# Optimization experiments

Measured on AMD Instinct MI355X. Metric: run time of the kernel, lower is better.

Reference implementation:

```python
import jax, jax.numpy as jnp
import numpy as np

OVERLAP_THRESH = 0.5
NEG_POS_RATIO = 3
VARIANCE = (0.1, 0.2)


def point_form(boxes):
    # center-size (cx,cy,w,h) -> corner (xmin,ymin,xmax,ymax)
    return jnp.concatenate([boxes[:, :2] - boxes[:, 2:] / 2,
                            boxes[:, :2] + boxes[:, 2:] / 2], axis=1)


def jaccard(a, b):
    # a: [O,4] corner boxes, b: [P,4] corner boxes -> IoU [O,P]
    lt = jnp.maximum(a[:, None, :2], b[None, :, :2])
    rb = jnp.minimum(a[:, None, 2:], b[None, :, 2:])
    wh = jnp.clip(rb - lt, 0.0)
    inter = wh[..., 0] * wh[..., 1]
    area_a = (a[:, 2] - a[:, 0]) * (a[:, 3] - a[:, 1])
    area_b = (b[:, 2] - b[:, 0]) * (b[:, 3] - b[:, 1])
    return inter / (area_a[:, None] + area_b[None, :] - inter)


def match_one(truths, priors):
    # truths: [O,4] corner form; priors: [P,4] center-size form
    O = truths.shape[0]
    overlaps = jaccard(truths, point_form(priors))          # [O,P]
    best_prior_idx = jnp.argmax(overlaps, axis=1)           # [O]
    best_truth_overlap = jnp.max(overlaps, axis=0)          # [P]
    best_truth_idx = jnp.argmax(overlaps, axis=0)           # [P]
    # force-assign each gt its best prior
    best_truth_overlap = best_truth_overlap.at[best_prior_idx].set(2.0)
    best_truth_idx = best_truth_idx.at[best_prior_idx].set(jnp.arange(O))
    matches = truths[best_truth_idx]                        # [P,4]
    # ARM: labels are all zeros -> conf = 0 + 1 = 1 for matched, 0 otherwise
    conf = jnp.where(best_truth_overlap < OVERLAP_THRESH, 0, 1).astype(jnp.int32)
    # encode(matched, priors, variances)
    g_cxcy = ((matches[:, :2] + matches[:, 2:]) / 2 - priors[:, :2]) / (VARIANCE[0] * priors[:, 2:])
    g_wh = jnp.log((matches[:, 2:] - matches[:, :2]) / priors[:, 2:]) / VARIANCE[1]
    loc = jnp.concatenate([g_cxcy, g_wh], axis=1)           # [P,4]
    return loc, conf


def arm_loss(loc_data, conf_data, priors, targets):
    B, P, _ = loc_data.shape
    truths = targets[:, :, :4]                              # [B,O,4]
    loc_t, conf_t = jax.vmap(lambda t: match_one(t, priors))(truths)
    loc_t = jax.lax.stop_gradient(loc_t)                    # match targets are detached
    conf_t = jax.lax.stop_gradient(conf_t)
    pos = conf_t > 0                                        # [B,P]

    # localization loss: smooth L1 over positive priors, sum reduction
    diff = loc_data - loc_t
    ad = jnp.abs(diff)
    sl1 = jnp.where(ad < 1.0, 0.5 * diff * diff, ad - 0.5)
    loss_l = jnp.sum(sl1 * pos[..., None].astype(loc_data.dtype))

    # per-prior CE for mining and final loss
    lse = jax.nn.logsumexp(conf_data, axis=-1)              # [B,P]
    c_gt = jnp.take_along_axis(conf_data, conf_t[..., None], axis=-1)[..., 0]
    ce = lse - c_gt                                         # [B,P]

    # hard negative mining: rank negatives by CE (positives zeroed out)
    rank_src = jax.lax.stop_gradient(jnp.where(pos, 0.0, ce))
    loss_idx = jnp.argsort(-rank_src, axis=1)
    idx_rank = jnp.argsort(loss_idx, axis=1)
    num_pos = jnp.sum(pos.astype(jnp.int32), axis=1, keepdims=True)  # [B,1]
    num_neg = jnp.minimum(NEG_POS_RATIO * num_pos, P - 1)
    neg = idx_rank < num_neg                                # [B,P]

    mask = (pos | neg).astype(conf_data.dtype)
    loss_c = jnp.sum(ce * mask)

    N = jnp.sum(num_pos).astype(loc_data.dtype)
    return loss_l / N, loss_c / N


def setup_inputs() -> dict:
    key = jax.random.key(0)
    k1, k2, k3, k4, k5, k6 = jax.random.split(key, 6)
    B, P, O = 64, 32768, 16
    loc_data = jax.random.normal(k1, (B, P, 4), dtype=jnp.float32)
    conf_data = jax.random.normal(k2, (B, P, 2), dtype=jnp.float32)
    # priors: center-size form, interior centers, positive w/h
    cxcy = jax.random.uniform(k3, (P, 2), minval=0.05, maxval=0.95)
    wh = jax.random.uniform(k4, (P, 2), minval=0.02, maxval=0.30)
    priors = jnp.concatenate([cxcy, wh], axis=1).astype(jnp.float32)
    # targets: valid corner-form gt boxes with positive area + label column
    c = jax.random.uniform(k5, (B, O, 2), minval=0.1, maxval=0.9)
    s = jax.random.uniform(k6, (B, O, 2), minval=0.05, maxval=0.4)
    mn = jnp.clip(c - s / 2, 0.0, 1.0)
    mx = jnp.clip(c + s / 2, 0.0, 1.0)
    labels = jnp.ones((B, O, 1), dtype=jnp.float32)
    targets = jnp.concatenate([mn, mx, labels], axis=2).astype(jnp.float32)
    return {"loc_data": loc_data, "conf_data": conf_data, "priors": priors, "targets": targets}


def reference(loc_data, conf_data, priors, targets):
    return arm_loss(loc_data, conf_data, priors, targets)
```

## Files before the change

kernel.cpp:

```cpp
#include <hip/hip_runtime.h>
#include <stdint.h>

#define B_ 64
#define P_ 32768
#define O_ 16
#define BP_CHUNK 1024
#define MATCH_BLOCKS (P_ / 512 * B_)

constexpr float OVERLAP_THRESH = 0.5f;
constexpr int   NEG_POS_RATIO  = 3;
constexpr float VAR0 = 0.1f;
constexpr float VAR1 = 0.2f;

__device__ __forceinline__ unsigned long long umax64(unsigned long long a,
                                                     unsigned long long b) {
    return a > b ? a : b;
}

__global__ __launch_bounds__(256)
void best_prior_kernel(const float* __restrict__ priors,
                       const float* __restrict__ targets,
                       unsigned long long* __restrict__ bp_pack) {
    int b   = blockIdx.y;
    int tid = threadIdx.x;
    int g   = tid >> 4;
    int o   = tid & 15;

    const float* t = targets + ((size_t)b * O_ + o) * 5;
    float tx0 = t[0], ty0 = t[1], tx1 = t[2], ty1 = t[3];
    float ta  = (tx1 - tx0) * (ty1 - ty0);

    int pbase = blockIdx.x * BP_CHUNK + g;
    float bin_ = 0.f, bun_ = 1.f;
    int   bp_  = pbase;

    #pragma unroll 4
    for (int j = 0; j < BP_CHUNK / 16; ++j) {
        int p = pbase + j * 16;
        float4 pr = ((const float4*)priors)[p];
        float px0 = pr.x - pr.z * 0.5f, py0 = pr.y - pr.w * 0.5f;
        float px1 = pr.x + pr.z * 0.5f, py1 = pr.y + pr.w * 0.5f;
        float pa  = (px1 - px0) * (py1 - py0);
        float w = fmaxf(fminf(tx1, px1) - fmaxf(tx0, px0), 0.f);
        float h = fmaxf(fminf(ty1, py1) - fmaxf(ty0, py0), 0.f);
        float in_ = w * h;
        float un_ = ta + pa - in_;
        bool gt = in_ * bun_ > bin_ * un_;
        bin_ = gt ? in_ : bin_;
        bun_ = gt ? un_ : bun_;
        bp_  = gt ? p   : bp_;
    }

    float iou = bin_ / bun_;
    unsigned long long pack =
        ((unsigned long long)__float_as_uint(iou) << 32) | (unsigned)(~bp_);

    pack = umax64(pack, __shfl_xor(pack, 16, 64));
    pack = umax64(pack, __shfl_xor(pack, 32, 64));

    __shared__ unsigned long long sw[4][16];
    int lane = tid & 63, wid = tid >> 6;
    if (lane < 16) sw[wid][lane] = pack;
    __syncthreads();
    if (tid < 16) {
        unsigned long long m = umax64(umax64(sw[0][tid], sw[1][tid]),
                                      umax64(sw[2][tid], sw[3][tid]));
        atomicMax(&bp_pack[(size_t)b * O_ + tid], m);
    }
}

__device__ __forceinline__ float sl1(float d) {
    float ad = fabsf(d);
    return (ad < 1.f) ? 0.5f * d * d : ad - 0.5f;
}

__global__ __launch_bounds__(256)
void match_kernel(const float* __restrict__ loc_data,
                  const float* __restrict__ conf_data,
                  const float* __restrict__ priors,
                  const float* __restrict__ targets,
                  const unsigned* __restrict__ bp_lo,
                  float* __restrict__ rank,
                  int* __restrict__ num_pos,
                  float2* __restrict__ blk_part) {
    int b    = blockIdx.y;
    int tid  = threadIdx.x;
    int pair = blockIdx.x * 256 + tid;
    int p0   = pair * 2;
    const float* tb = targets + (size_t)b * O_ * 5;

    float4 prA = ((const float4*)priors)[p0];
    float4 prB = ((const float4*)priors)[p0 + 1];
    float4 cd  = ((const float4*)conf_data)[(size_t)b * (P_ / 2) + pair];

    float ax0 = prA.x - prA.z * 0.5f, ay0 = prA.y - prA.w * 0.5f;
    float ax1 = prA.x + prA.z * 0.5f, ay1 = prA.y + prA.w * 0.5f;
    float bx0 = prB.x - prB.z * 0.5f, by0 = prB.y - prB.w * 0.5f;
    float bx1 = prB.x + prB.z * 0.5f, by1 = prB.y + prB.w * 0.5f;
    float aA = (ax1 - ax0) * (ay1 - ay0);
    float aB = (bx1 - bx0) * (by1 - by0);

    float ibA = 0.f, ubA = 1.f, ibB = 0.f, ubB = 1.f;
    int miA = 0, miB = 0, fiA = -1, fiB = -1;

    #pragma unroll
    for (int o = 0; o < O_; ++o) {
        float tx0 = tb[o * 5 + 0], ty0 = tb[o * 5 + 1];
        float tx1 = tb[o * 5 + 2], ty1 = tb[o * 5 + 3];
        float ta  = (tx1 - tx0) * (ty1 - ty0);
        int   bp  = (int)~bp_lo[((size_t)b * O_ + o) * 2];

        float wA  = fmaxf(fminf(tx1, ax1) - fmaxf(tx0, ax0), 0.f);
        float hA  = fmaxf(fminf(ty1, ay1) - fmaxf(ty0, ay0), 0.f);
        float inA = wA * hA;
        float unA = ta + aA - inA;
        bool  gA  = inA * ubA > ibA * unA;
        ibA = gA ? inA : ibA;  ubA = gA ? unA : ubA;  miA = gA ? o : miA;
        if (bp == p0) fiA = o;

        float wB  = fmaxf(fminf(tx1, bx1) - fmaxf(tx0, bx0), 0.f);
        float hB  = fmaxf(fminf(ty1, by1) - fmaxf(ty0, by0), 0.f);
        float inB = wB * hB;
        float unB = ta + aB - inB;
        bool  gB  = inB * ubB > ibB * unB;
        ibB = gB ? inB : ibB;  ubB = gB ? unB : ubB;  miB = gB ? o : miB;
        if (bp == p0 + 1) fiB = o;
    }

    bool posA = (fiA >= 0) || (2.f * ibA >= ubA);
    bool posB = (fiB >= 0) || (2.f * ibB >= ubB);

    float mA  = fmaxf(cd.x, cd.y);
    float ceA = mA + __logf(1.f + __expf(-fabsf(cd.x - cd.y))) - (posA ? cd.y : cd.x);
    float mB  = fmaxf(cd.z, cd.w);
    float ceB = mB + __logf(1.f + __expf(-fabsf(cd.z - cd.w))) - (posB ? cd.w : cd.z);

    float2 rk;
    rk.x = posA ? 0.f : ceA;
    rk.y = posB ? 0.f : ceB;
    *(float2*)(rank + (size_t)b * P_ + p0) = rk;

    float ll = 0.f, ces = 0.f;
    int   pc = 0;

    if (posA) {
        int mi = (fiA >= 0) ? fiA : miA;
        float mx0 = tb[mi * 5 + 0], my0 = tb[mi * 5 + 1];
        float mx1 = tb[mi * 5 + 2], my1 = tb[mi * 5 + 3];
        float pz = ax1 - ax0, pw = ay1 - ay0;
        float cx = (ax0 + ax1) * 0.5f, cy = (ay0 + ay1) * 0.5f;
        float gcx = ((mx0 + mx1) * 0.5f - cx) / (VAR0 * pz);
        float gcy = ((my0 + my1) * 0.5f - cy) / (VAR0 * pw);
        float gw  = __logf((mx1 - mx0) / pz) * (1.f / VAR1);
        float gh  = __logf((my1 - my0) / pw) * (1.f / VAR1);
        float4 ld = ((const float4*)loc_data)[(size_t)b * P_ + p0];
        ll  += sl1(ld.x - gcx) + sl1(ld.y - gcy) + sl1(ld.z - gw) + sl1(ld.w - gh);
        ces += ceA;
        pc  += 1;
    }
    if (posB) {
        int mi = (fiB >= 0) ? fiB : miB;
        float mx0 = tb[mi * 5 + 0], my0 = tb[mi * 5 + 1];
        float mx1 = tb[mi * 5 + 2], my1 = tb[mi * 5 + 3];
        float pz = bx1 - bx0, pw = by1 - by0;
        float cx = (bx0 + bx1) * 0.5f, cy = (by0 + by1) * 0.5f;
        float gcx = ((mx0 + mx1) * 0.5f - cx) / (VAR0 * pz);
        float gcy = ((my0 + my1) * 0.5f - cy) / (VAR0 * pw);
        float gw  = __logf((mx1 - mx0) / pz) * (1.f / VAR1);
        float gh  = __logf((my1 - my0) / pw) * (1.f / VAR1);
        float4 ld = ((const float4*)loc_data)[(size_t)b * P_ + p0 + 1];
        ll  += sl1(ld.x - gcx) + sl1(ld.y - gcy) + sl1(ld.z - gw) + sl1(ld.w - gh);
        ces += ceB;
        pc  += 1;
    }

    for (int off = 32; off; off >>= 1) {
        ll  += __shfl_down(ll, off, 64);
        ces += __shfl_down(ces, off, 64);
        pc  += __shfl_down(pc, off, 64);
    }
    __shared__ float sll[4], sce[4];
    __shared__ int   spc[4];
    int wid = tid >> 6;
    if ((tid & 63) == 0) { sll[wid] = ll; sce[wid] = ces; spc[wid] = pc; }
    __syncthreads();
    if (tid == 0) {
        int tp = spc[0] + spc[1] + spc[2] + spc[3];
        float tl = sll[0] + sll[1] + sll[2] + sll[3];
        float tc = sce[0] + sce[1] + sce[2] + sce[3];
        blk_part[blockIdx.y * gridDim.x + blockIdx.x] = make_float2(tl, tc);
        if (tp) atomicAdd(&num_pos[b], tp);
    }
}

__global__ __launch_bounds__(1024)
void topk_kernel(const float* __restrict__ rank,
                 const int* __restrict__ num_pos,
                 double* __restrict__ acc) {
    int b   = blockIdx.x;
    int tid = threadIdx.x;
    int np  = num_pos[b];
    int k   = min(NEG_POS_RATIO * np, P_ - 1);
    if (k <= 0) return;

    const uint4* r4 = (const uint4*)(rank + (size_t)b * P_);
    unsigned key[32];
    #pragma unroll
    for (int j = 0; j < 8; ++j) {
        uint4 v = r4[j * 1024 + tid];
        key[j * 4 + 0] = v.x; key[j * 4 + 1] = v.y;
        key[j * 4 + 2] = v.z; key[j * 4 + 3] = v.w;
    }

    __shared__ unsigned cnt[2048];
    __shared__ unsigned wsum[16];
    __shared__ unsigned s_pre;
    __shared__ int      s_k;

    int lane = tid & 63, wid = tid >> 6;
    unsigned pre = 0;
    int kk = k;

    #pragma unroll
    for (int level = 0; level < 3; ++level) {
        const int shift = (level == 0) ? 21 : (level == 1) ? 10 : 0;
        const int hishf = (level == 1) ? 21 : 10;
        const unsigned fmask = (level == 2) ? 0x3FFu : 0x7FFu;
        const int nb = (level == 2) ? 1024 : 2048;

        cnt[tid] = 0; cnt[tid + 1024] = 0;
        __syncthreads();

        if (level == 0) {
            #pragma unroll
            for (int j = 0; j < 32; ++j)
                atomicAdd(&cnt[key[j] >> 21], 1u);
        } else {
            #pragma unroll
            for (int j = 0; j < 32; ++j) {
                unsigned u = key[j];
                if ((u >> hishf) == pre) atomicAdd(&cnt[(u >> shift) & fmask], 1u);
            }
        }
        __syncthreads();

        unsigned c1 = (2 * tid + 1 < nb) ? cnt[2 * tid + 1] : 0u;
        unsigned c0 = ((2 * tid < nb) ? cnt[2 * tid] : 0u) + c1;
        unsigned g = c0, G = g;
        #pragma unroll
        for (int off = 1; off < 64; off <<= 1) {
            unsigned r = __shfl_down(G, off, 64);
            if (lane + off < 64) G += r;
        }
        if (lane == 0) wsum[wid] = G;
        __syncthreads();
        unsigned T = 0;
        for (int w = wid + 1; w < 16; ++w) T += wsum[w];
        unsigned A  = (G - g) + T;
        unsigned S1 = A + c1;
        unsigned S0 = A + c0;
        unsigned ukk = (unsigned)kk;
        if (2 * tid + 1 < nb && S1 >= ukk && A < ukk) {
            s_pre = (unsigned)(2 * tid + 1); s_k = kk - (int)A;
        } else if (2 * tid < nb && S0 >= ukk && S1 < ukk) {
            s_pre = (unsigned)(2 * tid);     s_k = kk - (int)S1;
        }
        __syncthreads();
        pre = (pre << ((level == 2) ? 10 : 11)) | s_pre;
        kk  = s_k;
        __syncthreads();
    }

    unsigned kth = pre;
    double sum = 0.0;
    int cg = 0;
    #pragma unroll
    for (int j = 0; j < 32; ++j) {
        unsigned u = key[j];
        if (u > kth) { sum += (double)__uint_as_float(u); ++cg; }
    }
    for (int off = 32; off; off >>= 1) {
        sum += __shfl_down(sum, off, 64);
        cg  += __shfl_down(cg, off, 64);
    }
    __shared__ double ssum[16];
    __shared__ int    scg[16];
    if (lane == 0) { ssum[wid] = sum; scg[wid] = cg; }
    __syncthreads();
    if (tid == 0) {
        double tsum = 0.0; int tcg = 0;
        for (int i = 0; i < 16; ++i) { tsum += ssum[i]; tcg += scg[i]; }
        double total = tsum + (double)(k - tcg) * (double)__uint_as_float(kth);
        atomicAdd(&acc[2], total);
    }
}

__global__ __launch_bounds__(1024)
void finalize_kernel(const float2* __restrict__ blk_part,
                     const int* __restrict__ num_pos,
                     const double* __restrict__ acc,
                     float* __restrict__ out) {
    int tid = threadIdx.x;
    double ll = 0.0, ce = 0.0;
    #pragma unroll
    for (int j = 0; j < MATCH_BLOCKS / 1024; ++j) {
        float2 v = blk_part[j * 1024 + tid];
        ll += (double)v.x;
        ce += (double)v.y;
    }
    int n = (tid < B_) ? num_pos[tid] : 0;

    int lane = tid & 63, wid = tid >> 6;
    for (int off = 32; off; off >>= 1) {
        ll += __shfl_down(ll, off, 64);
        ce += __shfl_down(ce, off, 64);
        n  += __shfl_down(n, off, 64);
    }
    __shared__ double sll[16], sce[16];
    __shared__ int    sn[16];
    if (lane == 0) { sll[wid] = ll; sce[wid] = ce; sn[wid] = n; }
    __syncthreads();
    if (tid == 0) {
        double tll = 0.0, tce = 0.0; int tn = 0;
        for (int i = 0; i < 16; ++i) { tll += sll[i]; tce += sce[i]; tn += sn[i]; }
        double Nd = (double)tn;
        out[0] = (float)(tll / Nd);
        out[1] = (float)((tce + acc[2]) / Nd);
    }
}

extern "C" void kernel_launch(void* const* d_in, const int* in_sizes, int n_in,
                              void* d_out, int out_size, void* d_ws, size_t ws_size,
                              hipStream_t stream) {
    const float* loc_data  = (const float*)d_in[0];
    const float* conf_data = (const float*)d_in[1];
    const float* priors    = (const float*)d_in[2];
    const float* targets   = (const float*)d_in[3];

    char* ws = (char*)d_ws;
    unsigned long long* bp_pack = (unsigned long long*)ws;
    int*    num_pos  = (int*)(ws + 8192);
    double* acc      = (double*)(ws + 8192 + 256);
    float2* blk_part = (float2*)(ws + 16384);
    float*  rank     = (float*)(ws + 65536);

    hipMemsetAsync(ws, 0, 8192 + 512, stream);

    best_prior_kernel<<<dim3(P_ / BP_CHUNK, B_), 256, 0, stream>>>(
        priors, targets, bp_pack);
    match_kernel<<<dim3(P_ / 512, B_), 256, 0, stream>>>(
        loc_data, conf_data, priors, targets, (const unsigned*)bp_pack,
        rank, num_pos, blk_part);
    topk_kernel<<<B_, 1024, 0, stream>>>(rank, num_pos, acc);
    finalize_kernel<<<1, 1024, 0, stream>>>(blk_part, num_pos, acc, (float*)d_out);
}
```

Before: 85.67 us.

## Stage target boxes in LDS and fuse finalize into topk via last-block ticket

The match kernel now loads the 16 target boxes, their areas and the best-prior indices into shared memory once per block, rather than re-reading them from global memory inside the unrolled loop. The finalize kernel is removed. The last topk block to finish, found with an atomic ticket counter and threadfences, does the final reduction, so one kernel launch is saved. Per-batch top-k totals are written to a slot array instead of being added atomically into one double, which makes the final sum order deterministic.

```diff
diff --git a/kernel.cpp b/kernel.cpp
--- a/kernel.cpp
+++ b/kernel.cpp
@@ -87,7 +87,17 @@
     int tid  = threadIdx.x;
     int pair = blockIdx.x * 256 + tid;
     int p0   = pair * 2;
-    const float* tb = targets + (size_t)b * O_ * 5;
+
+    __shared__ float4 s_box[O_];
+    __shared__ float2 s_meta[O_];
+    if (tid < O_) {
+        const float* t = targets + ((size_t)b * O_ + tid) * 5;
+        float x0 = t[0], y0 = t[1], x1 = t[2], y1 = t[3];
+        s_box[tid]  = make_float4(x0, y0, x1, y1);
+        int bp = (int)~bp_lo[((size_t)b * O_ + tid) * 2];
+        s_meta[tid] = make_float2((x1 - x0) * (y1 - y0), __int_as_float(bp));
+    }
+    __syncthreads();
 
     float4 prA = ((const float4*)priors)[p0];
     float4 prB = ((const float4*)priors)[p0 + 1];
@@ -105,10 +115,11 @@
 
     #pragma unroll
     for (int o = 0; o < O_; ++o) {
-        float tx0 = tb[o * 5 + 0], ty0 = tb[o * 5 + 1];
-        float tx1 = tb[o * 5 + 2], ty1 = tb[o * 5 + 3];
-        float ta  = (tx1 - tx0) * (ty1 - ty0);
-        int   bp  = (int)~bp_lo[((size_t)b * O_ + o) * 2];
+        float4 tb4 = s_box[o];
+        float2 mt  = s_meta[o];
+        float tx0 = tb4.x, ty0 = tb4.y, tx1 = tb4.z, ty1 = tb4.w;
+        float ta  = mt.x;
+        int   bp  = __float_as_int(mt.y);
 
         float wA  = fmaxf(fminf(tx1, ax1) - fmaxf(tx0, ax0), 0.f);
         float hA  = fmaxf(fminf(ty1, ay1) - fmaxf(ty0, ay0), 0.f);
@@ -145,14 +156,13 @@
 
     if (posA) {
         int mi = (fiA >= 0) ? fiA : miA;
-        float mx0 = tb[mi * 5 + 0], my0 = tb[mi * 5 + 1];
-        float mx1 = tb[mi * 5 + 2], my1 = tb[mi * 5 + 3];
+        float4 tb4 = s_box[mi];
         float pz = ax1 - ax0, pw = ay1 - ay0;
         float cx = (ax0 + ax1) * 0.5f, cy = (ay0 + ay1) * 0.5f;
-        float gcx = ((mx0 + mx1) * 0.5f - cx) / (VAR0 * pz);
-        float gcy = ((my0 + my1) * 0.5f - cy) / (VAR0 * pw);
-        float gw  = __logf((mx1 - mx0) / pz) * (1.f / VAR1);
-        float gh  = __logf((my1 - my0) / pw) * (1.f / VAR1);
+        float gcx = ((tb4.x + tb4.z) * 0.5f - cx) / (VAR0 * pz);
+        float gcy = ((tb4.y + tb4.w) * 0.5f - cy) / (VAR0 * pw);
+        float gw  = __logf((tb4.z - tb4.x) / pz) * (1.f / VAR1);
+        float gh  = __logf((tb4.w - tb4.y) / pw) * (1.f / VAR1);
         float4 ld = ((const float4*)loc_data)[(size_t)b * P_ + p0];
         ll  += sl1(ld.x - gcx) + sl1(ld.y - gcy) + sl1(ld.z - gw) + sl1(ld.w - gh);
         ces += ceA;
@@ -160,14 +170,13 @@
     }
     if (posB) {
         int mi = (fiB >= 0) ? fiB : miB;
-        float mx0 = tb[mi * 5 + 0], my0 = tb[mi * 5 + 1];
-        float mx1 = tb[mi * 5 + 2], my1 = tb[mi * 5 + 3];
+        float4 tb4 = s_box[mi];
         float pz = bx1 - bx0, pw = by1 - by0;
         float cx = (bx0 + bx1) * 0.5f, cy = (by0 + by1) * 0.5f;
-        float gcx = ((mx0 + mx1) * 0.5f - cx) / (VAR0 * pz);
-        float gcy = ((my0 + my1) * 0.5f - cy) / (VAR0 * pw);
-        float gw  = __logf((mx1 - mx0) / pz) * (1.f / VAR1);
-        float gh  = __logf((my1 - my0) / pw) * (1.f / VAR1);
+        float gcx = ((tb4.x + tb4.z) * 0.5f - cx) / (VAR0 * pz);
+        float gcy = ((tb4.y + tb4.w) * 0.5f - cy) / (VAR0 * pw);
+        float gw  = __logf((tb4.z - tb4.x) / pz) * (1.f / VAR1);
+        float gh  = __logf((tb4.w - tb4.y) / pw) * (1.f / VAR1);
         float4 ld = ((const float4*)loc_data)[(size_t)b * P_ + p0 + 1];
         ll  += sl1(ld.x - gcx) + sl1(ld.y - gcy) + sl1(ld.z - gw) + sl1(ld.w - gh);
         ces += ceB;
@@ -196,111 +205,117 @@
 __global__ __launch_bounds__(1024)
 void topk_kernel(const float* __restrict__ rank,
                  const int* __restrict__ num_pos,
-                 double* __restrict__ acc) {
+                 const float2* __restrict__ blk_part,
+                 unsigned long long* __restrict__ blk_topk,
+                 unsigned* __restrict__ counter,
+                 float* __restrict__ out) {
     int b   = blockIdx.x;
     int tid = threadIdx.x;
     int np  = num_pos[b];
     int k   = min(NEG_POS_RATIO * np, P_ - 1);
-    if (k <= 0) return;
-
-    const uint4* r4 = (const uint4*)(rank + (size_t)b * P_);
-    unsigned key[32];
-    #pragma unroll
-    for (int j = 0; j < 8; ++j) {
-        uint4 v = r4[j * 1024 + tid];
-        key[j * 4 + 0] = v.x; key[j * 4 + 1] = v.y;
-        key[j * 4 + 2] = v.z; key[j * 4 + 3] = v.w;
-    }
 
     __shared__ unsigned cnt[2048];
     __shared__ unsigned wsum[16];
     __shared__ unsigned s_pre;
     __shared__ int      s_k;
-
+    __shared__ unsigned s_ticket;
     int lane = tid & 63, wid = tid >> 6;
-    unsigned pre = 0;
-    int kk = k;
-
-    #pragma unroll
-    for (int level = 0; level < 3; ++level) {
-        const int shift = (level == 0) ? 21 : (level == 1) ? 10 : 0;
-        const int hishf = (level == 1) ? 21 : 10;
-        const unsigned fmask = (level == 2) ? 0x3FFu : 0x7FFu;
-        const int nb = (level == 2) ? 1024 : 2048;
-
-        cnt[tid] = 0; cnt[tid + 1024] = 0;
+
+    double total = 0.0;
+    if (k > 0) {
+        const uint4* r4 = (const uint4*)(rank + (size_t)b * P_);
+        unsigned key[32];
+        #pragma unroll
+        for (int j = 0; j < 8; ++j) {
+            uint4 v = r4[j * 1024 + tid];
+            key[j * 4 + 0] = v.x; key[j * 4 + 1] = v.y;
+            key[j * 4 + 2] = v.z; key[j * 4 + 3] = v.w;
+        }
+
+        unsigned pre = 0;
+        int kk = k;
+        #pragma unroll
+        for (int level = 0; level < 3; ++level) {
+            const int shift = (level == 0) ? 21 : (level == 1) ? 10 : 0;
+            const int hishf = (level == 1) ? 21 : 10;
+            const unsigned fmask = (level == 2) ? 0x3FFu : 0x7FFu;
+            const int nb = (level == 2) ? 1024 : 2048;
+
+            cnt[tid] = 0; cnt[tid + 1024] = 0;
+            __syncthreads();
+
+            if (level == 0) {
+                #pragma unroll
+                for (int j = 0; j < 32; ++j)
+                    atomicAdd(&cnt[key[j] >> 21], 1u);
+            } else {
+                #pragma unroll
+                for (int j = 0; j < 32; ++j) {
+                    unsigned u = key[j];
+                    if ((u >> hishf) == pre) atomicAdd(&cnt[(u >> shift) & fmask], 1u);
+                }
+            }
+            __syncthreads();
+
+            unsigned c1 = (2 * tid + 1 < nb) ? cnt[2 * tid + 1] : 0u;
+            unsigned c0 = ((2 * tid < nb) ? cnt[2 * tid] : 0u) + c1;
+            unsigned g = c0, G = g;
+            #pragma unroll
+            for (int off = 1; off < 64; off <<= 1) {
+                unsigned r = __shfl_down(G, off, 64);
+                if (lane + off < 64) G += r;
+            }
+            if (lane == 0) wsum[wid] = G;
+            __syncthreads();
+            unsigned T = 0;
+            for (int w = wid + 1; w < 16; ++w) T += wsum[w];
+            unsigned A  = (G - g) + T;
+            unsigned S1 = A + c1;
+            unsigned S0 = A + c0;
+            unsigned ukk = (unsigned)kk;
+            if (2 * tid + 1 < nb && S1 >= ukk && A < ukk) {
+                s_pre = (unsigned)(2 * tid + 1); s_k = kk - (int)A;
+            } else if (2 * tid < nb && S0 >= ukk && S1 < ukk) {
+                s_pre = (unsigned)(2 * tid);     s_k = kk - (int)S1;
+            }
+            __syncthreads();
+            pre = (pre << ((level == 2) ? 10 : 11)) | s_pre;
+            kk  = s_k;
+            __syncthreads();
+        }
+
+        unsigned kth = pre;
+        double sum = 0.0;
+        int cg = 0;
+        #pragma unroll
+        for (int j = 0; j < 32; ++j) {
+            unsigned u = key[j];
+            if (u > kth) { sum += (double)__uint_as_float(u); ++cg; }
+        }
+        for (int off = 32; off; off >>= 1) {
+            sum += __shfl_down(sum, off, 64);
+            cg  += __shfl_down(cg, off, 64);
+        }
+        __shared__ double ssum[16];
+        __shared__ int    scg[16];
+        if (lane == 0) { ssum[wid] = sum; scg[wid] = cg; }
         __syncthreads();
-
-        if (level == 0) {
-            #pragma unroll
-            for (int j = 0; j < 32; ++j)
-                atomicAdd(&cnt[key[j] >> 21], 1u);
-        } else {
-            #pragma unroll
-            for (int j = 0; j < 32; ++j) {
-                unsigned u = key[j];
-                if ((u >> hishf) == pre) atomicAdd(&cnt[(u >> shift) & fmask], 1u);
-            }
-        }
-        __syncthreads();
-
-        unsigned c1 = (2 * tid + 1 < nb) ? cnt[2 * tid + 1] : 0u;
-        unsigned c0 = ((2 * tid < nb) ? cnt[2 * tid] : 0u) + c1;
-        unsigned g = c0, G = g;
-        #pragma unroll
-        for (int off = 1; off < 64; off <<= 1) {
-            unsigned r = __shfl_down(G, off, 64);
-            if (lane + off < 64) G += r;
-        }
-        if (lane == 0) wsum[wid] = G;
-        __syncthreads();
-        unsigned T = 0;
-        for (int w = wid + 1; w < 16; ++w) T += wsum[w];
-        unsigned A  = (G - g) + T;
-        unsigned S1 = A + c1;
-        unsigned S0 = A + c0;
-        unsigned ukk = (unsigned)kk;
-        if (2 * tid + 1 < nb && S1 >= ukk && A < ukk) {
-            s_pre = (unsigned)(2 * tid + 1); s_k = kk - (int)A;
-        } else if (2 * tid < nb && S0 >= ukk && S1 < ukk) {
-            s_pre = (unsigned)(2 * tid);     s_k = kk - (int)S1;
-        }
-        __syncthreads();
-        pre = (pre << ((level == 2) ? 10 : 11)) | s_pre;
-        kk  = s_k;
-        __syncthreads();
-    }
-
-    unsigned kth = pre;
-    double sum = 0.0;
-    int cg = 0;
-    #pragma unroll
-    for (int j = 0; j < 32; ++j) {
-        unsigned u = key[j];
-        if (u > kth) { sum += (double)__uint_as_float(u); ++cg; }
-    }
-    for (int off = 32; off; off >>= 1) {
-        sum += __shfl_down(sum, off, 64);
-        cg  += __shfl_down(cg, off, 64);
-    }
-    __shared__ double ssum[16];
-    __shared__ int    scg[16];
-    if (lane == 0) { ssum[wid] = sum; scg[wid] = cg; }
-    __syncthreads();
+        if (tid == 0) {
+            double tsum = 0.0; int tcg = 0;
+            for (int i = 0; i < 16; ++i) { tsum += ssum[i]; tcg += scg[i]; }
+            total = tsum + (double)(k - tcg) * (double)__uint_as_float(kth);
+        }
+    }
+
     if (tid == 0) {
-        double tsum = 0.0; int tcg = 0;
-        for (int i = 0; i < 16; ++i) { tsum += ssum[i]; tcg += scg[i]; }
-        double total = tsum + (double)(k - tcg) * (double)__uint_as_float(kth);
-        atomicAdd(&acc[2], total);
-    }
-}
-
-__global__ __launch_bounds__(1024)
-void finalize_kernel(const float2* __restrict__ blk_part,
-                     const int* __restrict__ num_pos,
-                     const double* __restrict__ acc,
-                     float* __restrict__ out) {
-    int tid = threadIdx.x;
+        atomicExch(&blk_topk[b], (unsigned long long)__double_as_longlong(total));
+        __threadfence();
+        s_ticket = atomicAdd(counter, 1u);
+    }
+    __syncthreads();
+    if (s_ticket != B_ - 1) return;
+
+    __threadfence();
     double ll = 0.0, ce = 0.0;
     #pragma unroll
     for (int j = 0; j < MATCH_BLOCKS / 1024; ++j) {
@@ -309,23 +324,28 @@
         ce += (double)v.y;
     }
     int n = (tid < B_) ? num_pos[tid] : 0;
-
-    int lane = tid & 63, wid = tid >> 6;
+    double tk = (tid < B_)
+        ? __longlong_as_double((long long)atomicAdd(&blk_topk[tid], 0ull))
+        : 0.0;
+
     for (int off = 32; off; off >>= 1) {
         ll += __shfl_down(ll, off, 64);
         ce += __shfl_down(ce, off, 64);
+        tk += __shfl_down(tk, off, 64);
         n  += __shfl_down(n, off, 64);
     }
-    __shared__ double sll[16], sce[16];
-    __shared__ int    sn[16];
-    if (lane == 0) { sll[wid] = ll; sce[wid] = ce; sn[wid] = n; }
+    __shared__ double fll[16], fce[16], ftk[16];
+    __shared__ int    fn[16];
+    if (lane == 0) { fll[wid] = ll; fce[wid] = ce; ftk[wid] = tk; fn[wid] = n; }
     __syncthreads();
     if (tid == 0) {
-        double tll = 0.0, tce = 0.0; int tn = 0;
-        for (int i = 0; i < 16; ++i) { tll += sll[i]; tce += sce[i]; tn += sn[i]; }
+        double tll = 0.0, tce = 0.0, ttk = 0.0; int tn = 0;
+        for (int i = 0; i < 16; ++i) {
+            tll += fll[i]; tce += fce[i]; ttk += ftk[i]; tn += fn[i];
+        }
         double Nd = (double)tn;
         out[0] = (float)(tll / Nd);
-        out[1] = (float)((tce + acc[2]) / Nd);
+        out[1] = (float)((tce + ttk) / Nd);
     }
 }
 
@@ -338,19 +358,20 @@
     const float* targets   = (const float*)d_in[3];
 
     char* ws = (char*)d_ws;
-    unsigned long long* bp_pack = (unsigned long long*)ws;
-    int*    num_pos  = (int*)(ws + 8192);
-    double* acc      = (double*)(ws + 8192 + 256);
-    float2* blk_part = (float2*)(ws + 16384);
-    float*  rank     = (float*)(ws + 65536);
-
-    hipMemsetAsync(ws, 0, 8192 + 512, stream);
+    unsigned long long* bp_pack  = (unsigned long long*)ws;
+    int*                num_pos  = (int*)(ws + 8192);
+    unsigned*           counter  = (unsigned*)(ws + 8448);
+    unsigned long long* blk_topk = (unsigned long long*)(ws + 8704);
+    float2*             blk_part = (float2*)(ws + 16384);
+    float*              rank     = (float*)(ws + 65536);
+
+    hipMemsetAsync(ws, 0, 8512, stream);
 
     best_prior_kernel<<<dim3(P_ / BP_CHUNK, B_), 256, 0, stream>>>(
         priors, targets, bp_pack);
     match_kernel<<<dim3(P_ / 512, B_), 256, 0, stream>>>(
         loc_data, conf_data, priors, targets, (const unsigned*)bp_pack,
         rank, num_pos, blk_part);
-    topk_kernel<<<B_, 1024, 0, stream>>>(rank, num_pos, acc);
-    finalize_kernel<<<1, 1024, 0, stream>>>(blk_part, num_pos, acc, (float*)d_out);
-}
+    topk_kernel<<<B_, 1024, 0, stream>>>(rank, num_pos, blk_part, blk_topk,
+                                         counter, (float*)d_out);
+}
```

Result: no change. 87.00 us (+1.6%).
